# Kernel tuning notes

Hardware: AMD Instinct MI355X
Metric: run time of the kernel (lower is better)

Reference implementation:

```python
import jax, jax.numpy as jnp
import numpy as np
from jax import lax

EPS = 1e-7  # keras K.epsilon()
DN = ('NHWC', 'HWIO', 'NHWC')


def _box_avg(z, k):
    """Depthwise k x k box filter with SAME padding, scaled by 1/(k*k*C).
    Matches tf.nn.depthwise_conv2d with a ones/(k*k*C) kernel, implemented
    separably (two 1D convs) for efficiency."""
    C = z.shape[-1]
    scale = 1.0 / (k * k * C)  # note: keras code divides by full kernel size incl. C
    kh = jnp.ones((k, 1, 1, C), z.dtype)
    kw = jnp.ones((1, k, 1, C), z.dtype)
    z = lax.conv_general_dilated(z, kh, (1, 1), 'SAME',
                                 dimension_numbers=DN, feature_group_count=C)
    z = lax.conv_general_dilated(z, kw, (1, 1), 'SAME',
                                 dimension_numbers=DN, feature_group_count=C)
    return z * scale


def setup_inputs() -> dict:
    key = jax.random.key(0)
    x = jax.random.normal(key, (8, 1024, 1024, 2), dtype=jnp.float32)
    return {"x": x, "filter_size": 61}


def reference(x, filter_size):
    k = int(filter_size)
    # norm_method == 'std':
    out = x - _box_avg(x, k)                       # local mean-subtract
    c1 = _box_avg(out, k)
    c2 = _box_avg(out * out, k)
    std = jnp.sqrt(c2 - c1 * c1) + EPS             # local window std
    return out / std
```

## Files before the change

### kernel.cpp

```cpp
#include <hip/hip_runtime.h>
#include <hip/hip_fp16.h>
#include <math.h>

#define NB 8
#define HH 1024
#define WW 1024
#define RAD 30
#define KS 61
#define ROWSZ 2048
#define IMGSZ (HH * ROWSZ)
#define STR2 1024
#define STR4 512
#define NCOL4 (NB * STR4)
#define VSEGH 32
#define VNSEG (HH / VSEGH)
#define EPSV 1e-7f
#define SCALEV (1.0f / (float)(KS * KS * 2))
#define PDW (WW + WW / 8)
#define PD(i) ((i) + ((i) >> 3))

#define MEMFENCE asm volatile("" ::: "memory")

__device__ __forceinline__ unsigned bf16_rn(float f) {
    unsigned u = __float_as_uint(f);
    return (u + 0x7FFFu + ((u >> 16) & 1u)) >> 16;
}
__device__ __forceinline__ unsigned pk2(float a, float b) {
    return bf16_rn(a) | (bf16_rn(b) << 16);
}
__device__ __forceinline__ float2 up2(unsigned u) {
    return make_float2(__uint_as_float(u << 16),
                       __uint_as_float(u & 0xFFFF0000u));
}
__device__ __forceinline__ unsigned pkh(float a, float b) {
    __half2 h = __floats2half2_rn(a, b);
    return *reinterpret_cast<unsigned*>(&h);
}
__device__ __forceinline__ float2 uph(unsigned u) {
    __half2 h = *reinterpret_cast<__half2*>(&u);
    return __half22float2(h);
}
__device__ __forceinline__ float2 f2add(float2 a, float2 b) {
    return make_float2(a.x + b.x, a.y + b.y);
}
__device__ __forceinline__ float2 f2sub(float2 a, float2 b) {
    return make_float2(a.x - b.x, a.y - b.y);
}
__device__ __forceinline__ float sqrt_f(float x) { return __builtin_amdgcn_sqrtf(x); }
__device__ __forceinline__ float rcp_f(float x)  { return __builtin_amdgcn_rcpf(x); }

__global__ __launch_bounds__(256, 2) void vbox_kernel(const float* __restrict__ in,
                                                      unsigned* __restrict__ out) {
    int tid = blockIdx.x * 256 + threadIdx.x;
    int col = tid & (NCOL4 - 1);
    int seg = tid >> 12;
    int n = col >> 9;
    int c = col & (STR4 - 1);
    const float4* ip = (const float4*)(in + (size_t)n * IMGSZ) + c;
    uint2* op = (uint2*)(out + (size_t)n * (IMGSZ / 2)) + c;
    int h0 = seg * VSEGH;
    float4 S = make_float4(0.f, 0.f, 0.f, 0.f);
    int lo = h0 - RAD; if (lo < 0) lo = 0;
    int hiend = h0 + RAD; if (hiend > HH) hiend = HH;
    int h = lo;
    for (; h + 16 <= hiend; h += 16) {
        float4 W[16];
        #pragma unroll
        for (int i = 0; i < 16; ++i) W[i] = ip[(h + i) * STR4];
        MEMFENCE;
        #pragma unroll
        for (int i = 0; i < 16; ++i) {
            S.x += W[i].x; S.y += W[i].y; S.z += W[i].z; S.w += W[i].w;
        }
    }
    for (; h + 8 <= hiend; h += 8) {
        float4 W[8];
        #pragma unroll
        for (int i = 0; i < 8; ++i) W[i] = ip[(h + i) * STR4];
        MEMFENCE;
        #pragma unroll
        for (int i = 0; i < 8; ++i) {
            S.x += W[i].x; S.y += W[i].y; S.z += W[i].z; S.w += W[i].w;
        }
    }
    for (; h < hiend; ++h) {
        float4 w = ip[h * STR4];
        S.x += w.x; S.y += w.y; S.z += w.z; S.w += w.w;
    }

    if (h0 >= RAD && h0 + VSEGH + RAD <= HH) {
        const float4* lp = ip + (h0 + RAD) * STR4;
        const float4* tp = ip + (h0 - RAD) * STR4;
        uint2* opp = op + (size_t)h0 * STR4;
        float4 LA[8], TA[8], LB[8], TB[8], LC[8], TC[8];
#define VB_LOAD(Lx, Tx, r) { \
        _Pragma("unroll") for (int i = 0; i < 8; ++i) Lx[i] = lp[((r) + i) * STR4]; \
        _Pragma("unroll") for (int i = 0; i < 8; ++i) Tx[i] = tp[((r) + i) * STR4]; \
        MEMFENCE; }
#define VB_CONS(Lx, Tx, r) { \
        _Pragma("unroll") for (int i = 0; i < 8; ++i) { \
            S.x += Lx[i].x; S.y += Lx[i].y; S.z += Lx[i].z; S.w += Lx[i].w; \
            opp[((r) + i) * STR4] = make_uint2(pk2(S.x, S.y), pk2(S.z, S.w)); \
            S.x -= Tx[i].x; S.y -= Tx[i].y; S.z -= Tx[i].z; S.w -= Tx[i].w; } }
        VB_LOAD(LA, TA, 0)
        VB_LOAD(LB, TB, 8)
        VB_LOAD(LC, TC, 16)
        VB_CONS(LA, TA, 0)
        VB_LOAD(LA, TA, 24)
        VB_CONS(LB, TB, 8)
        VB_CONS(LC, TC, 16)
        VB_CONS(LA, TA, 24)
#undef VB_LOAD
#undef VB_CONS
    } else {
        const float4 Z = make_float4(0.f, 0.f, 0.f, 0.f);
        for (int ho = h0; ho < h0 + VSEGH; ho += 4) {
            float4 a[4], b[4];
            #pragma unroll
            for (int i = 0; i < 4; ++i) {
                int ha = ho + i + RAD;
                a[i] = (ha < HH) ? ip[ha * STR4] : Z;
            }
            #pragma unroll
            for (int i = 0; i < 4; ++i) {
                int hb = ho + i - RAD;
                b[i] = (hb >= 0) ? ip[hb * STR4] : Z;
            }
            #pragma unroll
            for (int i = 0; i < 4; ++i) {
                S.x += a[i].x; S.y += a[i].y; S.z += a[i].z; S.w += a[i].w;
                op[(size_t)(ho + i) * STR4] = make_uint2(pk2(S.x, S.y), pk2(S.z, S.w));
                S.x -= b[i].x; S.y -= b[i].y; S.z -= b[i].z; S.w -= b[i].w;
            }
        }
    }
}

__device__ inline float wave_incl_scan(float v) {
    int lane = threadIdx.x & 63;
    #pragma unroll
    for (int d = 1; d < 64; d <<= 1) {
        float o = __shfl_up(v, d, 64);
        if (lane >= d) v += o;
    }
    return v;
}

__global__ __launch_bounds__(256) void hmid_kernel(const unsigned* __restrict__ vsum,
                                                   const float* __restrict__ x,
                                                   unsigned* __restrict__ oh,
                                                   uint2* __restrict__ hig) {
    __shared__ float ch[2][PDW];
    __shared__ float s4[4][PDW];
    __shared__ float wtot[4];
    int t = threadIdx.x;
    size_t g = (size_t)blockIdx.x * ROWSZ;
    const uint4* vrow = (const uint4*)(vsum + (size_t)blockIdx.x * STR2);
    uint4 u = vrow[t];
    {
        float2 p0 = up2(u.x), p1 = up2(u.y), p2 = up2(u.z), p3 = up2(u.w);
        int w = 4 * t;
        ch[0][PD(w + 0)] = p0.x; ch[1][PD(w + 0)] = p0.y;
        ch[0][PD(w + 1)] = p1.x; ch[1][PD(w + 1)] = p1.y;
        ch[0][PD(w + 2)] = p2.x; ch[1][PD(w + 2)] = p2.y;
        ch[0][PD(w + 3)] = p3.x; ch[1][PD(w + 3)] = p3.y;
    }
    __syncthreads();
    {
        int c = t >> 7, j = t & 127, base = j * 8;
        float v[8]; float run = 0.f;
        #pragma unroll
        for (int i = 0; i < 8; ++i) { run += ch[c][PD(base + i)]; v[i] = run; }
        float incl = wave_incl_scan(run);
        int wid = t >> 6;
        if ((t & 63) == 63) wtot[wid] = incl;
        __syncthreads();
        float off = incl - run;
        if (wid & 1) off += wtot[wid - 1];
        #pragma unroll
        for (int i = 0; i < 8; ++i) ch[c][PD(base + i)] = off + v[i];
    }
    __syncthreads();
    const float4* xrow = (const float4*)(x + g);
    uint2* ohrow = (uint2*)(oh + (size_t)blockIdx.x * STR2);
    #pragma unroll
    for (int i = 0; i < 2; ++i) {
        int jj = t + 256 * i;
        int w0 = 2 * jj, w1 = 2 * jj + 1;
        int hi0 = w0 + RAD; if (hi0 > WW - 1) hi0 = WW - 1;
        int hi1 = w1 + RAD; if (hi1 > WW - 1) hi1 = WW - 1;
        int lo0 = w0 - RAD - 1, lo1 = w1 - RAD - 1;
        float s00 = ch[0][PD(hi0)], s10 = ch[1][PD(hi0)];
        if (lo0 >= 0) { s00 -= ch[0][PD(lo0)]; s10 -= ch[1][PD(lo0)]; }
        float s01 = ch[0][PD(hi1)], s11 = ch[1][PD(hi1)];
        if (lo1 >= 0) { s01 -= ch[0][PD(lo1)]; s11 -= ch[1][PD(lo1)]; }
        float4 xv = xrow[jj];
        float4 o;
        o.x = xv.x - SCALEV * s00; o.y = xv.y - SCALEV * s10;
        o.z = xv.z - SCALEV * s01; o.w = xv.w - SCALEV * s11;
        ohrow[jj] = make_uint2(pkh(o.x, o.y), pkh(o.z, o.w));
        s4[0][PD(w0)] = o.x;       s4[1][PD(w0)] = o.y;
        s4[0][PD(w1)] = o.z;       s4[1][PD(w1)] = o.w;
        s4[2][PD(w0)] = o.x * o.x; s4[3][PD(w0)] = o.y * o.y;
        s4[2][PD(w1)] = o.z * o.z; s4[3][PD(w1)] = o.w * o.w;
    }
    __syncthreads();
    {
        int a = t >> 6, j = t & 63, base = j * 16;
        float v[16]; float run = 0.f;
        #pragma unroll
        for (int i = 0; i < 16; ++i) { run += s4[a][PD(base + i)]; v[i] = run; }
        float incl = wave_incl_scan(run);
        float off = incl - run;
        #pragma unroll
        for (int i = 0; i < 16; ++i) s4[a][PD(base + i)] = off + v[i];
    }
    __syncthreads();
    uint4* hirow = (uint4*)(hig + (size_t)blockIdx.x * STR2);
    #pragma unroll
    for (int i = 0; i < 2; ++i) {
        int jj = t + 256 * i;
        int w0 = 2 * jj, w1 = 2 * jj + 1;
        int hi0 = w0 + RAD; if (hi0 > WW - 1) hi0 = WW - 1;
        int hi1 = w1 + RAD; if (hi1 > WW - 1) hi1 = WW - 1;
        int lo0 = w0 - RAD - 1, lo1 = w1 - RAD - 1;
        float a00 = s4[0][PD(hi0)], a10 = s4[1][PD(hi0)];
        float q00 = s4[2][PD(hi0)], q10 = s4[3][PD(hi0)];
        if (lo0 >= 0) {
            a00 -= s4[0][PD(lo0)]; a10 -= s4[1][PD(lo0)];
            q00 -= s4[2][PD(lo0)]; q10 -= s4[3][PD(lo0)];
        }
        float a01 = s4[0][PD(hi1)], a11 = s4[1][PD(hi1)];
        float q01 = s4[2][PD(hi1)], q11 = s4[3][PD(hi1)];
        if (lo1 >= 0) {
            a01 -= s4[0][PD(lo1)]; a11 -= s4[1][PD(lo1)];
            q01 -= s4[2][PD(lo1)]; q11 -= s4[3][PD(lo1)];
        }
        hirow[jj] = make_uint4(pk2(a00, a10), pk2(q00, q10),
                               pk2(a01, a11), pk2(q01, q11));
    }
}

__global__ __launch_bounds__(256, 2) void vfinal_kernel(const uint2* __restrict__ hi,
                                                        const unsigned* __restrict__ oh,
                                                        float* __restrict__ fout) {
    int tid = blockIdx.x * 256 + threadIdx.x;
    int col = tid & (NCOL4 - 1);
    int seg = tid >> 12;
    int n = col >> 9;
    int c = col & (STR4 - 1);
    const uint4* pp = (const uint4*)(hi + (size_t)n * (size_t)HH * STR2) + c;
    const uint2* po = (const uint2*)(oh + (size_t)n * (IMGSZ / 2)) + c;
    float4* fo = (float4*)(fout + (size_t)n * IMGSZ) + c;
    int h0 = seg * VSEGH;
    float2 S1a = make_float2(0.f, 0.f), S2a = make_float2(0.f, 0.f);
    float2 S1b = make_float2(0.f, 0.f), S2b = make_float2(0.f, 0.f);
    int lo = h0 - RAD; if (lo < 0) lo = 0;
    int hiend = h0 + RAD; if (hiend > HH) hiend = HH;
    int h = lo;
    for (; h + 8 <= hiend; h += 8) {
        uint4 A[8];
        #pragma unroll
        for (int i = 0; i < 8; ++i) A[i] = pp[(h + i) * STR4];
        MEMFENCE;
        #pragma unroll
        for (int i = 0; i < 8; ++i) {
            S1a = f2add(S1a, up2(A[i].x)); S2a = f2add(S2a, up2(A[i].y));
            S1b = f2add(S1b, up2(A[i].z)); S2b = f2add(S2b, up2(A[i].w));
        }
    }
    for (; h < hiend; ++h) {
        uint4 v = pp[h * STR4];
        S1a = f2add(S1a, up2(v.x)); S2a = f2add(S2a, up2(v.y));
        S1b = f2add(S1b, up2(v.z)); S2b = f2add(S2b, up2(v.w));
    }

#define VF_ROW(Ai, Oi, Ti, ro) { \
    S1a = f2add(S1a, up2((Ai).x)); S2a = f2add(S2a, up2((Ai).y)); \
    S1b = f2add(S1b, up2((Ai).z)); S2b = f2add(S2b, up2((Ai).w)); \
    float2 oA = uph((Oi).x), oB = uph((Oi).y); \
    float4 yv; \
    yv.x = oA.x * rcp_f(sqrt_f(fmaxf(SCALEV * S2a.x - (SCALEV * S1a.x) * (SCALEV * S1a.x), 0.f)) + EPSV); \
    yv.y = oA.y * rcp_f(sqrt_f(fmaxf(SCALEV * S2a.y - (SCALEV * S1a.y) * (SCALEV * S1a.y), 0.f)) + EPSV); \
    yv.z = oB.x * rcp_f(sqrt_f(fmaxf(SCALEV * S2b.x - (SCALEV * S1b.x) * (SCALEV * S1b.x), 0.f)) + EPSV); \
    yv.w = oB.y * rcp_f(sqrt_f(fmaxf(SCALEV * S2b.y - (SCALEV * S1b.y) * (SCALEV * S1b.y), 0.f)) + EPSV); \
    oq[(ro) * STR4] = yv; \
    S1a = f2sub(S1a, up2((Ti).x)); S2a = f2sub(S2a, up2((Ti).y)); \
    S1b = f2sub(S1b, up2((Ti).z)); S2b = f2sub(S2b, up2((Ti).w)); \
}

    if (h0 >= RAD && h0 + VSEGH + RAD <= HH) {
        const uint4* lp = pp + (h0 + RAD) * STR4;
        const uint4* tp = pp + (h0 - RAD) * STR4;
        const uint2* orp = po + (size_t)h0 * STR4;
        float4* oq = fo + (size_t)h0 * STR4;
        uint4 LA[8], TA[8], LB[8], TB[8];
        uint2 OA[8], OB[8];
#define VF_LOAD(Lx, Tx, Ox, r) { \
        _Pragma("unroll") for (int i = 0; i < 8; ++i) Lx[i] = lp[((r) + i) * STR4]; \
        _Pragma("unroll") for (int i = 0; i < 8; ++i) Tx[i] = tp[((r) + i) * STR4]; \
        _Pragma("unroll") for (int i = 0; i < 8; ++i) Ox[i] = orp[((r) + i) * STR4]; \
        MEMFENCE; }
#define VF_CONS(Lx, Tx, Ox, r) { \
        _Pragma("unroll") for (int i = 0; i < 8; ++i) VF_ROW(Lx[i], Ox[i], Tx[i], (r) + i) }
        VF_LOAD(LA, TA, OA, 0)
        VF_LOAD(LB, TB, OB, 8)
        VF_CONS(LA, TA, OA, 0)
        VF_LOAD(LA, TA, OA, 16)
        VF_CONS(LB, TB, OB, 8)
        VF_LOAD(LB, TB, OB, 24)
        VF_CONS(LA, TA, OA, 16)
        VF_CONS(LB, TB, OB, 24)
#undef VF_LOAD
#undef VF_CONS
    } else {
        const uint4 Z4 = make_uint4(0u, 0u, 0u, 0u);
        float4* oq = fo;
        for (int ho = h0; ho < h0 + VSEGH; ho += 4) {
            uint4 a[4], b[4];
            uint2 O[4];
            #pragma unroll
            for (int i = 0; i < 4; ++i) {
                int ha = ho + i + RAD;
                a[i] = (ha < HH) ? pp[ha * STR4] : Z4;
            }
            #pragma unroll
            for (int i = 0; i < 4; ++i) {
                int hb = ho + i - RAD;
                b[i] = (hb >= 0) ? pp[hb * STR4] : Z4;
            }
            #pragma unroll
            for (int i = 0; i < 4; ++i) O[i] = po[(size_t)(ho + i) * STR4];
            #pragma unroll
            for (int i = 0; i < 4; ++i) {
                VF_ROW(a[i], O[i], b[i], (size_t)(ho + i))
            }
        }
        (void)oq;
    }
#undef VF_ROW
}

extern "C" void kernel_launch(void* const* d_in, const int* in_sizes, int n_in,
                              void* d_out, int out_size, void* d_ws, size_t ws_size,
                              hipStream_t stream) {
    const float* x = (const float*)d_in[0];
    float* out = (float*)d_out;
    unsigned* V1 = (unsigned*)d_ws;
    unsigned* OH = V1;
    uint2* HI = (uint2*)(V1 + (size_t)NB * IMGSZ / 2);

    int vgrid = (NCOL4 * VNSEG) / 256;
    vbox_kernel<<<vgrid, 256, 0, stream>>>(x, V1);
    hmid_kernel<<<NB * HH, 256, 0, stream>>>(V1, x, OH, HI);
    vfinal_kernel<<<vgrid, 256, 0, stream>>>(HI, OH, out);
}
```

Measured before the change: 205.2 us.

## Stream vertical box-filter rows through per-wave LDS ring via global_load_lds

For interior segments, the vertical box kernel now prefetches input rows into a 16-slot per-wave LDS ring using direct global-to-LDS loads. The initial 60-row window sum and the 32-row sliding update both read from that ring while keeping about 14-20 loads in flight, paced by explicit vmcnt waits. This replaces register-array batching and is meant to deepen memory-level parallelism and cut VGPR pressure. It adds 64KB of LDS per block, which may limit occupancy. The hand-tuned waitcnt ordering and the dummy tail loads are fragile.

```diff
diff --git a/kernel.cpp b/kernel.cpp
--- a/kernel.cpp
+++ b/kernel.cpp
@@ -20,6 +20,14 @@
 #define PD(i) ((i) + ((i) >> 3))
 
 #define MEMFENCE asm volatile("" ::: "memory")
+#define WAITVM(N) asm volatile("s_waitcnt vmcnt(" #N ")" ::: "memory")
+#define WAITLGKM0 asm volatile("s_waitcnt lgkmcnt(0)" ::: "memory")
+
+__device__ __forceinline__ void glds16(const float4* g, char* l) {
+    __builtin_amdgcn_global_load_lds(
+        (const __attribute__((address_space(1))) void*)g,
+        (__attribute__((address_space(3))) void*)l, 16, 0, 0);
+}
 
 __device__ __forceinline__ unsigned bf16_rn(float f) {
     unsigned u = __float_as_uint(f);
@@ -51,6 +59,7 @@
 
 __global__ __launch_bounds__(256, 2) void vbox_kernel(const float* __restrict__ in,
                                                       unsigned* __restrict__ out) {
+    __shared__ __align__(16) char ring_lds[4][16][1024];
     int tid = blockIdx.x * 256 + threadIdx.x;
     int col = tid & (NCOL4 - 1);
     int seg = tid >> 12;
@@ -59,60 +68,78 @@
     const float4* ip = (const float4*)(in + (size_t)n * IMGSZ) + c;
     uint2* op = (uint2*)(out + (size_t)n * (IMGSZ / 2)) + c;
     int h0 = seg * VSEGH;
-    float4 S = make_float4(0.f, 0.f, 0.f, 0.f);
-    int lo = h0 - RAD; if (lo < 0) lo = 0;
-    int hiend = h0 + RAD; if (hiend > HH) hiend = HH;
-    int h = lo;
-    for (; h + 16 <= hiend; h += 16) {
-        float4 W[16];
-        #pragma unroll
-        for (int i = 0; i < 16; ++i) W[i] = ip[(h + i) * STR4];
-        MEMFENCE;
-        #pragma unroll
-        for (int i = 0; i < 16; ++i) {
-            S.x += W[i].x; S.y += W[i].y; S.z += W[i].z; S.w += W[i].w;
-        }
-    }
-    for (; h + 8 <= hiend; h += 8) {
-        float4 W[8];
-        #pragma unroll
-        for (int i = 0; i < 8; ++i) W[i] = ip[(h + i) * STR4];
-        MEMFENCE;
-        #pragma unroll
-        for (int i = 0; i < 8; ++i) {
-            S.x += W[i].x; S.y += W[i].y; S.z += W[i].z; S.w += W[i].w;
-        }
-    }
-    for (; h < hiend; ++h) {
-        float4 w = ip[h * STR4];
-        S.x += w.x; S.y += w.y; S.z += w.z; S.w += w.w;
-    }
 
     if (h0 >= RAD && h0 + VSEGH + RAD <= HH) {
-        const float4* lp = ip + (h0 + RAD) * STR4;
-        const float4* tp = ip + (h0 - RAD) * STR4;
+        int wv = threadIdx.x >> 6, lane = threadIdx.x & 63;
+        char* ringb = &ring_lds[wv][0][0];
+        int lo = h0 - RAD;
+        float4 S = make_float4(0.f, 0.f, 0.f, 0.f);
+
+        for (int s = 0; s < 16; ++s)
+            glds16(ip + (size_t)(lo + s) * STR4, ringb + s * 1024);
+
+        for (int j = 0; j < 44; ++j) {
+            WAITVM(14);
+            float4 v = *((const float4*)(ringb + (j & 15) * 1024) + lane);
+            WAITLGKM0; __builtin_amdgcn_sched_barrier(0);
+            glds16(ip + (size_t)(lo + 16 + j) * STR4, ringb + (j & 15) * 1024);
+            S.x += v.x; S.y += v.y; S.z += v.z; S.w += v.w;
+        }
+        for (int j = 44; j < 60; ++j) {
+            WAITVM(14);
+            float4 v = *((const float4*)(ringb + (j & 15) * 1024) + lane);
+            WAITLGKM0; __builtin_amdgcn_sched_barrier(0);
+            int d = j - 44;
+            const float4* wg; int ws;
+            if (d < 4)       { wg = ip + (size_t)(h0 - RAD + d) * STR4;        ws = 12 + d; }
+            else if (d < 12) { wg = ip + (size_t)(h0 + RAD + (d - 4)) * STR4;  ws = d - 4; }
+            else             { wg = ip + (size_t)(h0 - RAD + 4 + (d - 12)) * STR4; ws = 8 + (d - 12); }
+            glds16(wg, ringb + ws * 1024);
+            S.x += v.x; S.y += v.y; S.z += v.z; S.w += v.w;
+        }
+
         uint2* opp = op + (size_t)h0 * STR4;
-        float4 LA[8], TA[8], LB[8], TB[8], LC[8], TC[8];
-#define VB_LOAD(Lx, Tx, r) { \
-        _Pragma("unroll") for (int i = 0; i < 8; ++i) Lx[i] = lp[((r) + i) * STR4]; \
-        _Pragma("unroll") for (int i = 0; i < 8; ++i) Tx[i] = tp[((r) + i) * STR4]; \
-        MEMFENCE; }
-#define VB_CONS(Lx, Tx, r) { \
-        _Pragma("unroll") for (int i = 0; i < 8; ++i) { \
-            S.x += Lx[i].x; S.y += Lx[i].y; S.z += Lx[i].z; S.w += Lx[i].w; \
-            opp[((r) + i) * STR4] = make_uint2(pk2(S.x, S.y), pk2(S.z, S.w)); \
-            S.x -= Tx[i].x; S.y -= Tx[i].y; S.z -= Tx[i].z; S.w -= Tx[i].w; } }
-        VB_LOAD(LA, TA, 0)
-        VB_LOAD(LB, TB, 8)
-        VB_LOAD(LC, TC, 16)
-        VB_CONS(LA, TA, 0)
-        VB_LOAD(LA, TA, 24)
-        VB_CONS(LB, TB, 8)
-        VB_CONS(LC, TC, 16)
-        VB_CONS(LA, TA, 24)
-#undef VB_LOAD
-#undef VB_CONS
+        const float4* leadg = ip + (size_t)(h0 + RAD + 8) * STR4;
+        const float4* trailg = ip + (size_t)(h0 - RAD + 8) * STR4;
+#define VB_BODY(i)                                                              \
+        {                                                                       \
+            float4 lv = *((const float4*)(ringb + ((i) & 7) * 1024) + lane);    \
+            float4 tv = *((const float4*)(ringb + (8 + (((i) + 4) & 7)) * 1024) + lane); \
+            WAITLGKM0; __builtin_amdgcn_sched_barrier(0);                       \
+            if ((i) < 24) {                                                     \
+                glds16(leadg + (size_t)(i) * STR4, ringb + ((i) & 7) * 1024);   \
+                glds16(trailg + (size_t)(i) * STR4, ringb + (8 + (((i) + 4) & 7)) * 1024); \
+            } else {                                                            \
+                glds16(ip, ringb + ((i) & 7) * 1024);                           \
+                glds16(ip, ringb + ((i) & 7) * 1024);                           \
+            }                                                                   \
+            S.x += lv.x; S.y += lv.y; S.z += lv.z; S.w += lv.w;                 \
+            opp[(i) * STR4] = make_uint2(pk2(S.x, S.y), pk2(S.z, S.w));         \
+            S.x -= tv.x; S.y -= tv.y; S.z -= tv.z; S.w -= tv.w;                 \
+        }
+        for (int i = 0; i < 8; ++i)  { WAITVM(9);  VB_BODY(i) }
+        for (int i = 8; i < 24; ++i) { WAITVM(20); VB_BODY(i) }
+        for (int i = 24; i < 32; ++i){ WAITVM(20); VB_BODY(i) }
+#undef VB_BODY
     } else {
+        float4 S = make_float4(0.f, 0.f, 0.f, 0.f);
+        int lo = h0 - RAD; if (lo < 0) lo = 0;
+        int hiend = h0 + RAD; if (hiend > HH) hiend = HH;
+        int h = lo;
+        for (; h + 8 <= hiend; h += 8) {
+            float4 W[8];
+            #pragma unroll
+            for (int i = 0; i < 8; ++i) W[i] = ip[(h + i) * STR4];
+            MEMFENCE;
+            #pragma unroll
+            for (int i = 0; i < 8; ++i) {
+                S.x += W[i].x; S.y += W[i].y; S.z += W[i].z; S.w += W[i].w;
+            }
+        }
+        for (; h < hiend; ++h) {
+            float4 w = ip[h * STR4];
+            S.x += w.x; S.y += w.y; S.z += w.z; S.w += w.w;
+        }
         const float4 Z = make_float4(0.f, 0.f, 0.f, 0.f);
         for (int ho = h0; ho < h0 + VSEGH; ho += 4) {
             float4 a[4], b[4];
```

Measured after the change: 213.4 us. 1.04x slower.
